# Performance work log

Measured on AMD Instinct MI355X. Metric: run time of the kernel, lower is better.

The kernel has to match this reference:

```python
import jax, jax.numpy as jnp
import numpy as np

T_TOK, N_UNITS, E, H, L_PATH, N_PATHS, B, VOCAB = 16, 4096, 128, 128, 32, 1024, 8, 16384
MAX_PATH_LEN = 32
PAD_ID = 0


def _run_lstm(x, Wi, Wh, b):
    # x: [T, N, E]; torch gate order i, f, g, o
    Hh = Wh.shape[1]
    h0 = jnp.zeros((x.shape[1], Hh), x.dtype)
    def step(carry, xt):
        h, c = carry
        g = xt @ Wi.T + h @ Wh.T + b
        i, f, gg, o = jnp.split(g, 4, axis=-1)
        c = jax.nn.sigmoid(f) * c + jax.nn.sigmoid(i) * jnp.tanh(gg)
        h = jax.nn.sigmoid(o) * jnp.tanh(c)
        return (h, c), h
    _, ys = jax.lax.scan(step, (h0, h0), x)
    return ys


def _bilstm(x, lengths, Wif, Whf, bf, Wib, Whb, bb):
    # emulates pack_padded_sequence + bidirectional LSTM + pad_packed (zeros past length)
    T = x.shape[0]
    t = jnp.arange(T)[:, None]
    valid = t < lengths[None, :]
    out_f = _run_lstm(x, Wif, Whf, bf)
    rev = jnp.clip(lengths[None, :] - 1 - t, 0, T - 1)  # reverse within each valid prefix
    x_rev = jnp.take_along_axis(x, rev[:, :, None], axis=0)
    out_b = jnp.take_along_axis(_run_lstm(x_rev, Wib, Whb, bb), rev[:, :, None], axis=0)
    return jnp.concatenate([out_f, out_b], axis=-1) * valid[:, :, None]


def _layernorm(x, g, b):
    m = x.mean(-1, keepdims=True)
    v = ((x - m) ** 2).mean(-1, keepdims=True)
    return (x - m) * jax.lax.rsqrt(v + 1e-5) * g + b


def _forward(units, paths, unit_per_data, path_per_data, emb, tl_Wif, tl_Whf, tl_bf,
             tl_Wib, tl_Whb, tl_bb, lin_W, lin_b, ln_g, ln_b, attn_w, attn_b,
             pl_Wif, pl_Whf, pl_bf, pl_Wib, pl_Whb, pl_bb, ul_W, ul_b):
    # ---- _token_encoder ----
    is_pad = units == PAD_ID
    tok_len = jnp.where(is_pad.any(0), jnp.argmax(is_pad, 0), units.shape[0])
    x = emb[units]                                              # [T, NU, E]
    h = _bilstm(x, tok_len, tl_Wif, tl_Whf, tl_bf, tl_Wib, tl_Whb, tl_bb)  # [T, NU, 2H]
    out = h @ lin_W.T + lin_b                                   # [T, NU, E]
    q = jnp.tanh(_layernorm(out, ln_g, ln_b))
    scores = q @ attn_w.T + attn_b                              # [T, NU, 1] local attention
    scores = jnp.where(is_pad[:, :, None], -1e9, scores)
    w = jax.nn.softmax(scores, axis=0)
    tok_feat = jnp.einsum('tn,tne->ne', w[..., 0], out)         # [NU, E]
    # ---- _unit_to_path (vectorized ragged gather) ----
    Lp, Pn = paths.shape
    has_end = (paths == -1).any(0)
    fe = jnp.where(has_end, jnp.argmax(paths == -1, 0), Lp)
    ML = min(Lp, MAX_PATH_LEN)
    nb = unit_per_data.shape[0]
    data_of_path = jnp.repeat(jnp.arange(nb), path_per_data, total_repeat_length=Pn)
    u_off = jnp.cumsum(unit_per_data) - unit_per_data
    off_p = u_off[data_of_path]
    un_p = unit_per_data[data_of_path]
    pL = paths[:ML]
    t = jnp.arange(ML)[:, None]
    within = t < fe[None, :]
    keep = within & (pL >= 0) & (pL < un_p[None, :])
    gidx = jnp.clip(jnp.clip(pL, 0, None) + off_p[None, :], 0, tok_feat.shape[0] - 1)
    feats = tok_feat[gidx] * keep[:, :, None]                   # [ML, P, E]
    mask = jnp.where(within, (pL < 0) | (pL > un_p[None, :]), True)
    # ---- _path_encoder ----
    p_len = jnp.where(mask.any(0), jnp.argmax(mask, 0), ML)
    hp = _bilstm(feats, p_len, pl_Wif, pl_Whf, pl_bf, pl_Wib, pl_Whb, pl_bb)
    return hp @ ul_W.T + ul_b                                   # [ML, P, E]


def setup_inputs() -> dict:
    rng = np.random.default_rng(0)
    tok_len = rng.integers(4, T_TOK + 1, N_UNITS); tok_len[0] = T_TOK
    units = rng.integers(1, VOCAB, (T_TOK, N_UNITS))
    units = np.where(np.arange(T_TOK)[:, None] < tok_len[None, :], units, PAD_ID)
    upd = N_UNITS // B
    p_len = rng.integers(8, L_PATH + 1, N_PATHS); p_len[0] = L_PATH
    paths = rng.integers(0, upd, (L_PATH, N_PATHS))
    paths = np.where(np.arange(L_PATH)[:, None] < p_len[None, :], paths, -1)
    key = jax.random.key(0)
    ks = iter(jax.random.split(key, 24))
    def pn(shape, s=0.08):
        return (jax.random.normal(next(ks), shape) * s).astype(jnp.float32)
    return dict(
        units=jnp.asarray(units, jnp.int32),
        paths=jnp.asarray(paths, jnp.int32),
        unit_per_data=jnp.full((B,), upd, jnp.int32),
        path_per_data=jnp.full((B,), N_PATHS // B, jnp.int32),
        emb=pn((VOCAB, E)),
        tl_Wif=pn((4 * H, E)), tl_Whf=pn((4 * H, H)), tl_bf=pn((4 * H,)),
        tl_Wib=pn((4 * H, E)), tl_Whb=pn((4 * H, H)), tl_bb=pn((4 * H,)),
        lin_W=pn((E, 2 * H)), lin_b=pn((E,)),
        ln_g=jnp.ones((E,), jnp.float32), ln_b=jnp.zeros((E,), jnp.float32),
        attn_w=pn((1, E)), attn_b=pn((1,)),
        pl_Wif=pn((4 * H, E)), pl_Whf=pn((4 * H, H)), pl_bf=pn((4 * H,)),
        pl_Wib=pn((4 * H, E)), pl_Whb=pn((4 * H, H)), pl_bb=pn((4 * H,)),
        ul_W=pn((E, 2 * H)), ul_b=pn((E,)),
    )


def reference(units, paths, unit_per_data, path_per_data, emb, tl_Wif, tl_Whf, tl_bf,
              tl_Wib, tl_Whb, tl_bb, lin_W, lin_b, ln_g, ln_b, attn_w, attn_b,
              pl_Wif, pl_Whf, pl_bf, pl_Wib, pl_Whb, pl_bb, ul_W, ul_b):
    return _forward(units, paths, unit_per_data, path_per_data, emb, tl_Wif, tl_Whf, tl_bf,
                    tl_Wib, tl_Whb, tl_bb, lin_W, lin_b, ln_g, ln_b, attn_w, attn_b,
                    pl_Wif, pl_Whf, pl_bf, pl_Wib, pl_Whb, pl_bb, ul_W, ul_b)
```

## Files before the change

### kernel.cpp

```cpp
#include <hip/hip_runtime.h>
#include <cstdint>
#include <cstddef>

#define T_TOKN 16
#define NUNITS 4096
#define LPATH  32
#define NPATHS 1024
#define BNUM   8

typedef __attribute__((ext_vector_type(8))) short short8;
typedef __attribute__((ext_vector_type(4))) short short4x;
typedef __attribute__((ext_vector_type(4))) float f32x4;

enum : size_t {
  OFF_WFRAG   = 0,
  OFF_LINFRAG = 262144,
  OFF_OUTF    = 294912,
  OFF_OUTB    = OFF_OUTF + 4194304,
  OFF_OUTLIN  = OFF_OUTB + 4194304,
  OFF_SCORES  = OFF_OUTLIN + 8388608,
  OFF_TOKFEAT = OFF_SCORES + 65536,
  OFF_POUTF   = OFF_TOKFEAT + 524288,
  OFF_POUTB   = OFF_POUTF + 2097152,
  OFF_INT     = OFF_POUTB + 2097152,
  WS_FLOATS   = OFF_INT + 8192
};

static __device__ __forceinline__ unsigned short f2bf(float f) {
  union { float f; unsigned u; } v; v.f = f;
  unsigned r = v.u + 0x7fffu + ((v.u >> 16) & 1u);
  return (unsigned short)(r >> 16);
}
static __device__ __forceinline__ float bf2f(unsigned short u) {
  union { unsigned u; float f; } v; v.u = ((unsigned)u) << 16;
  return v.f;
}
static __device__ __forceinline__ float sigf(float x)      { return 1.f / (1.f + __expf(-x)); }
static __device__ __forceinline__ float tanhfast(float x)  { return 2.f / (1.f + __expf(-2.f * x)) - 1.f; }

__global__ void prep_kernel(
    const float* __restrict__ tWif, const float* __restrict__ tWhf,
    const float* __restrict__ tWib, const float* __restrict__ tWhb,
    const float* __restrict__ pWif, const float* __restrict__ pWhf,
    const float* __restrict__ pWib, const float* __restrict__ pWhb,
    const float* __restrict__ linW, const float* __restrict__ ulW,
    const int* __restrict__ units, const int* __restrict__ paths,
    const int* __restrict__ upd, const int* __restrict__ ppd,
    float* __restrict__ ws, int* __restrict__ ip)
{
  int idx = blockIdx.x * 256 + threadIdx.x;
  if (idx < 65536) {
    unsigned short* wf = (unsigned short*)(ws + OFF_WFRAG);
    int k8 = idx & 31, g = (idx >> 5) & 511, mat = idx >> 14;
    const float* Wi; const float* Wh;
    switch (mat) {
      case 0: Wi = tWif; Wh = tWhf; break;
      case 1: Wi = tWib; Wh = tWhb; break;
      case 2: Wi = pWif; Wh = pWhf; break;
      default: Wi = pWib; Wh = pWhb; break;
    }
    int kb = k8 << 3;
    const float* sp = (kb < 128) ? (Wi + g * 128 + kb) : (Wh + g * 128 + (kb - 128));
    float4 a = *(const float4*)sp;
    float4 b = *(const float4*)(sp + 4);
    int wvp = g >> 6, ct = (g >> 4) & 3, cl = g & 15;
    int ks = k8 >> 2, quad = k8 & 3;
    size_t base = ((size_t)mat << 17) +
                  (size_t)(((((wvp * 8 + ks) * 4 + ct) * 64) + quad * 16 + cl) << 3);
    short8 o;
    o[0] = (short)f2bf(a.x); o[1] = (short)f2bf(a.y);
    o[2] = (short)f2bf(a.z); o[3] = (short)f2bf(a.w);
    o[4] = (short)f2bf(b.x); o[5] = (short)f2bf(b.y);
    o[6] = (short)f2bf(b.z); o[7] = (short)f2bf(b.w);
    *(short8*)&wf[base] = o;
  } else if (idx < 65536 + 8192) {
    unsigned short* lf = (unsigned short*)(ws + OFF_LINFRAG);
    int j = idx - 65536;
    int k8 = j & 31, e = (j >> 5) & 127, mat = j >> 12;
    const float* W = mat ? ulW : linW;
    int kb = k8 << 3;
    const float* sp = W + e * 256 + kb;
    float4 a = *(const float4*)sp;
    float4 b = *(const float4*)(sp + 4);
    int ct = e >> 4, cl = e & 15;
    int ks = k8 >> 2, quad = k8 & 3;
    size_t base = ((size_t)mat << 15) +
                  (size_t)((((ct * 8 + ks) * 64) + quad * 16 + cl) << 3);
    short8 o;
    o[0] = (short)f2bf(a.x); o[1] = (short)f2bf(a.y);
    o[2] = (short)f2bf(a.z); o[3] = (short)f2bf(a.w);
    o[4] = (short)f2bf(b.x); o[5] = (short)f2bf(b.y);
    o[6] = (short)f2bf(b.z); o[7] = (short)f2bf(b.w);
    *(short8*)&lf[base] = o;
  } else if (idx < 73728 + 4096) {
    int n = idx - 73728;
    int len = T_TOKN;
    for (int t = 0; t < T_TOKN; ++t)
      if (units[t * NUNITS + n] == 0) { len = t; break; }
    ip[n] = len;
  } else if (idx < 77824 + 1024) {
    int p = idx - 77824;
    int* fe_a  = ip + 4096;
    int* p_len = ip + 5120;
    int* off_p = ip + 6144;
    int* un_p  = ip + 7168;
    int cum = 0; int d = BNUM - 1;
    for (int dd = 0; dd < BNUM; ++dd) {
      int c2 = cum + ppd[dd];
      if (p < c2) { d = dd; break; }
      cum = c2;
    }
    int off = 0;
    for (int dd = 0; dd < d; ++dd) off += upd[dd];
    int un = upd[d];
    off_p[p] = off; un_p[p] = un;
    int f = LPATH;
    for (int t = 0; t < LPATH; ++t)
      if (paths[t * NPATHS + p] == -1) { f = t; break; }
    fe_a[p] = f;
    int pl = LPATH;
    for (int t = 0; t < LPATH; ++t) {
      int v = paths[t * NPATHS + p];
      if ((t >= f) || (v < 0) || (v > un)) { pl = t; break; }
    }
    p_len[p] = pl;
  }
}

template <int MODE>
__global__ __launch_bounds__(1024, 4) void lstm_kernel(
    const unsigned short* __restrict__ wfragAll,
    const float* __restrict__ biasF, const float* __restrict__ biasB,
    const float* __restrict__ src,
    const int* __restrict__ idxsrc,
    const int* __restrict__ lens,
    const int* __restrict__ fe_a, const int* __restrict__ off_p, const int* __restrict__ un_p,
    unsigned short* __restrict__ outF, unsigned short* __restrict__ outB)
{
  constexpr int NN   = MODE ? NPATHS : NUNITS;
  constexpr int TT   = MODE ? LPATH : T_TOKN;
  constexpr int M    = MODE ? 8 : 32;
  constexpr int MR   = MODE ? 16 : 32;
  constexpr int NRT  = MR / 16;
  constexpr int ASTR = 264;
  constexpr int USTR = MODE ? 17 : 36;

  __shared__ unsigned short ash[MR * ASTR];
  __shared__ float gatesT[512 * USTR];
  __shared__ int   idxL[M * TT];

  int tid  = threadIdx.x;
  int dir  = blockIdx.y;
  int n0   = blockIdx.x * M;
  int lane = tid & 63, wv = tid >> 6;
  int cl   = lane & 15, quad = lane >> 4;

  const unsigned short* wbase =
      wfragAll + (size_t)((MODE ? 2 : 0) + dir) * 131072;
  int wv8 = wv >> 1;
  short8 bfr[8][2];
#pragma unroll
  for (int ks = 0; ks < 8; ++ks)
#pragma unroll
    for (int c2 = 0; c2 < 2; ++c2) {
      int ct = ((wv & 1) << 1) | c2;
      bfr[ks][c2] = *(const short8*)&wbase[((((wv8 * 8 + ks) * 4 + ct) * 64) + lane) * 8];
    }

  if (MODE == 0) {
    for (int i = tid; i < MR * 128; i += 1024)
      ash[(i >> 7) * ASTR + 128 + (i & 127)] = 0;
  } else {
    for (int i = tid; i < MR * ASTR; i += 1024) ash[i] = 0;
  }
  for (int i = tid; i < M * TT; i += 1024) {
    int u = i / TT, tt = i - u * TT;
    idxL[i] = idxsrc[tt * NN + (n0 + u)];
  }

  const float* bcp = dir ? biasB : biasF;
  const int jj  = tid & 127;
  const int ug  = tid >> 7;
  float bq[4];
#pragma unroll
  for (int q = 0; q < 4; ++q) bq[q] = bcp[q * 128 + jj];
  constexpr int NU = MODE ? 1 : 4;
  float cst[NU];
  int   ulen[NU];
#pragma unroll
  for (int i = 0; i < NU; ++i) {
    cst[i] = 0.f;
    ulen[i] = lens[n0 + ug * NU + i];
  }

  int gu, gk0;
  if (MODE == 0) { gu = tid >> 5; gk0 = (tid & 31) * 4; }
  else           { gu = tid >> 7; gk0 = tid & 127; }
  int gn = n0 + gu;
  int glen = lens[gn];
  int gfe = 0, goff = 0, gun = 0;
  if (MODE) { gfe = fe_a[gn]; goff = off_p[gn]; gun = un_p[gn]; }

  float4 xq; float xs;
  __syncthreads();

  {
    int tau = dir ? min(max(glen - 1, 0), TT - 1) : 0;
    int v = idxL[gu * TT + tau];
    if (MODE == 0) {
      xq = *(const float4*)&src[(size_t)v * 128 + gk0];
    } else {
      bool keep = (tau < gfe) && (v >= 0) && (v < gun);
      xs = keep ? src[(size_t)min(v + goff, NUNITS - 1) * 128 + gk0] : 0.f;
    }
  }
  if (MODE == 0) {
    short4x x4;
    x4[0] = (short)f2bf(xq.x); x4[1] = (short)f2bf(xq.y);
    x4[2] = (short)f2bf(xq.z); x4[3] = (short)f2bf(xq.w);
    *(short4x*)&ash[gu * ASTR + gk0] = x4;
  } else {
    ash[gu * ASTR + gk0] = f2bf(xs);
  }
  __syncthreads();

#pragma unroll 1
  for (int t = 0; t < TT; ++t) {
    {
      int tn = (t + 1 < TT) ? t + 1 : t;
      int taun = dir ? min(max(glen - 1 - tn, 0), TT - 1) : tn;
      int vn = idxL[gu * TT + taun];
      f32x4 acc[NRT][2];
#pragma unroll
      for (int rt = 0; rt < NRT; ++rt)
#pragma unroll
        for (int c2 = 0; c2 < 2; ++c2) {
          f32x4 z = {0.f, 0.f, 0.f, 0.f};
          acc[rt][c2] = z;
        }
#pragma unroll
      for (int ks = 0; ks < 8; ++ks) {
        short8 afr[NRT];
#pragma unroll
        for (int rt = 0; rt < NRT; ++rt)
          afr[rt] = *(const short8*)&ash[(rt * 16 + cl) * ASTR + ks * 32 + (quad << 3)];
#pragma unroll
        for (int rt = 0; rt < NRT; ++rt)
#pragma unroll
          for (int c2 = 0; c2 < 2; ++c2)
            acc[rt][c2] = __builtin_amdgcn_mfma_f32_16x16x32_bf16(
                afr[rt], bfr[ks][c2], acc[rt][c2], 0, 0, 0);
      }
      if (MODE == 0) {
        xq = *(const float4*)&src[(size_t)vn * 128 + gk0];
      } else {
        bool keep = (taun < gfe) && (vn >= 0) && (vn < gun);
        xs = keep ? src[(size_t)min(vn + goff, NUNITS - 1) * 128 + gk0] : 0.f;
      }
      if constexpr (MODE == 0) {
#pragma unroll
        for (int rt = 0; rt < NRT; ++rt)
#pragma unroll
          for (int c2 = 0; c2 < 2; ++c2) {
            int g = wv * 32 + c2 * 16 + cl;
            *(f32x4*)&gatesT[g * USTR + rt * 16 + (quad << 2)] = acc[rt][c2];
          }
      } else {
#pragma unroll
        for (int c2 = 0; c2 < 2; ++c2) {
          int g = wv * 32 + c2 * 16 + cl;
#pragma unroll
          for (int r = 0; r < 4; ++r)
            gatesT[g * USTR + (quad << 2) + r] = acc[0][c2][r];
        }
      }
    }
    __syncthreads();

    if constexpr (MODE == 0) {
      f32x4 gq0 = *(const f32x4*)&gatesT[(0 * 128 + jj) * USTR + (ug << 2)];
      f32x4 gq1 = *(const f32x4*)&gatesT[(1 * 128 + jj) * USTR + (ug << 2)];
      f32x4 gq2 = *(const f32x4*)&gatesT[(2 * 128 + jj) * USTR + (ug << 2)];
      f32x4 gq3 = *(const f32x4*)&gatesT[(3 * 128 + jj) * USTR + (ug << 2)];
#pragma unroll
      for (int r = 0; r < 4; ++r) {
        int u = (ug << 2) + r, n = n0 + u, L = ulen[r];
        if (t < L) {
          float iv = sigf(gq0[r] + bq[0]);
          float fv = sigf(gq1[r] + bq[1]);
          float gv = tanhfast(gq2[r] + bq[2]);
          float ov = sigf(gq3[r] + bq[3]);
          float c = fv * cst[r] + iv * gv;
          cst[r] = c;
          unsigned short hb = f2bf(ov * tanhfast(c));
          ash[u * ASTR + 128 + jj] = hb;
          if (dir == 0) outF[((size_t)t * NN + n) * 128 + jj] = hb;
          else          outB[((size_t)(L - 1 - t) * NN + n) * 128 + jj] = hb;
        } else {
          if (dir == 0) outF[((size_t)t * NN + n) * 128 + jj] = 0;
          else          outB[((size_t)t * NN + n) * 128 + jj] = 0;
        }
      }
    } else {
      int u = ug, n = n0 + u, L = ulen[0];
      if (t < L) {
        float p0 = gatesT[(0 * 128 + jj) * USTR + u] + bq[0];
        float p1 = gatesT[(1 * 128 + jj) * USTR + u] + bq[1];
        float p2 = gatesT[(2 * 128 + jj) * USTR + u] + bq[2];
        float p3 = gatesT[(3 * 128 + jj) * USTR + u] + bq[3];
        float ig = sigf(p0), fg = sigf(p1), gg = tanhfast(p2), og = sigf(p3);
        float c = fg * cst[0] + ig * gg;
        cst[0] = c;
        unsigned short hb = f2bf(og * tanhfast(c));
        ash[u * ASTR + 128 + jj] = hb;
        if (dir == 0) outF[((size_t)t * NN + n) * 128 + jj] = hb;
        else          outB[((size_t)(L - 1 - t) * NN + n) * 128 + jj] = hb;
      } else {
        if (dir == 0) outF[((size_t)t * NN + n) * 128 + jj] = 0;
        else          outB[((size_t)t * NN + n) * 128 + jj] = 0;
      }
    }
    if (t + 1 < TT) {
      if (MODE == 0) {
        short4x x4;
        x4[0] = (short)f2bf(xq.x); x4[1] = (short)f2bf(xq.y);
        x4[2] = (short)f2bf(xq.z); x4[3] = (short)f2bf(xq.w);
        *(short4x*)&ash[gu * ASTR + gk0] = x4;
      } else {
        ash[gu * ASTR + gk0] = f2bf(xs);
      }
    }
    __syncthreads();
  }
}

template <int EPI>
__global__ __launch_bounds__(256) void gemm_mfma(
    const unsigned short* __restrict__ INf, const unsigned short* __restrict__ INb,
    const int* __restrict__ lens,
    const unsigned short* __restrict__ Bfrag, const float* __restrict__ bias,
    void* __restrict__ OUTv, float* __restrict__ scores,
    const float* __restrict__ lng, const float* __restrict__ lnb,
    const float* __restrict__ attw, const float* __restrict__ attb,
    const int* __restrict__ units, int Nn)
{
  constexpr int OSTR = 132;
  __shared__ float outs[64 * OSTR];
  __shared__ float red1[256];
  __shared__ float red2[256];
  __shared__ float rowm[64], rowr[64];
  __shared__ float awsh[128], lgsh[128], lbsh[128];

  int tid = threadIdx.x, lane = tid & 63, wv = tid >> 6;
  int row0 = blockIdx.x * 64;
  int t = row0 / Nn, n0 = row0 % Nn;

  if (EPI == 1 && tid < 128) {
    awsh[tid] = attw[tid]; lgsh[tid] = lng[tid]; lbsh[tid] = lnb[tid];
  }

  short8 bfr[8][2];
#pragma unroll
  for (int ks = 0; ks < 8; ++ks)
#pragma unroll
    for (int c2 = 0; c2 < 2; ++c2) {
      int ct = wv * 2 + c2;
      bfr[ks][c2] = *(const short8*)&Bfrag[(((ct * 8 + ks) * 64) + lane) * 8];
    }

  int rb = lane & 15;
  int koq = (lane >> 4) << 3;
  bool val[4];
#pragma unroll
  for (int rt = 0; rt < 4; ++rt)
    val[rt] = (EPI == 1) ? true : (t < lens[n0 + rt * 16 + rb]);

  f32x4 acc[4][2];
#pragma unroll
  for (int rt = 0; rt < 4; ++rt)
#pragma unroll
    for (int c2 = 0; c2 < 2; ++c2) {
      f32x4 z = {0.f, 0.f, 0.f, 0.f};
      acc[rt][c2] = z;
    }

#pragma unroll
  for (int ks = 0; ks < 8; ++ks) {
    const unsigned short* P = (ks < 4) ? INf : INb;
    int koff = (ks & 3) * 32 + koq;
#pragma unroll
    for (int rt = 0; rt < 4; ++rt) {
      short8 a = {0, 0, 0, 0, 0, 0, 0, 0};
      if (val[rt])
        a = *(const short8*)&P[((size_t)(row0 + rt * 16 + rb)) * 128 + koff];
#pragma unroll
      for (int c2 = 0; c2 < 2; ++c2)
        acc[rt][c2] = __builtin_amdgcn_mfma_f32_16x16x32_bf16(
            a, bfr[ks][c2], acc[rt][c2], 0, 0, 0);
    }
  }

  float bc[2];
#pragma unroll
  for (int c2 = 0; c2 < 2; ++c2) bc[c2] = bias[wv * 32 + c2 * 16 + rb];
#pragma unroll
  for (int rt = 0; rt < 4; ++rt)
#pragma unroll
    for (int c2 = 0; c2 < 2; ++c2) {
      int col = wv * 32 + c2 * 16 + rb;
      int ub  = rt * 16 + ((lane >> 4) << 2);
#pragma unroll
      for (int r = 0; r < 4; ++r)
        outs[(ub + r) * OSTR + col] = acc[rt][c2][r] + bc[c2];
    }
  __syncthreads();

  int row = tid >> 2, seg = tid & 3;
  const float* rp = &outs[row * OSTR + seg * 32];
  size_t go = ((size_t)(row0 + row)) * 128 + seg * 32;

  if (EPI == 0) {
    float* OUT = (float*)OUTv;
#pragma unroll
    for (int x = 0; x < 8; ++x)
      *(f32x4*)&OUT[go + x * 4] = *(const f32x4*)&rp[x * 4];
  } else {
    unsigned short* OUT = (unsigned short*)OUTv;
    f32x4 v[8];
    float s = 0.f, s2 = 0.f;
#pragma unroll
    for (int x = 0; x < 8; ++x) {
      v[x] = *(const f32x4*)&rp[x * 4];
#pragma unroll
      for (int c = 0; c < 4; ++c) { s += v[x][c]; s2 += v[x][c] * v[x][c]; }
    }
    red1[tid] = s; red2[tid] = s2;
    __syncthreads();
    if (tid < 64) {
      float a = red1[tid * 4] + red1[tid * 4 + 1] + red1[tid * 4 + 2] + red1[tid * 4 + 3];
      float b = red2[tid * 4] + red2[tid * 4 + 1] + red2[tid * 4 + 2] + red2[tid * 4 + 3];
      float m = a * (1.f / 128.f);
      float var = b * (1.f / 128.f) - m * m;
      rowm[tid] = m;
      rowr[tid] = rsqrtf(var + 1e-5f);
    }
    __syncthreads();
    float m = rowm[row], rs = rowr[row];
    float sp = 0.f;
#pragma unroll
    for (int x = 0; x < 8; ++x) {
      short4x pv;
#pragma unroll
      for (int c = 0; c < 4; ++c) {
        int col = seg * 32 + x * 4 + c;
        float q = tanhfast((v[x][c] - m) * rs * lgsh[col] + lbsh[col]);
        sp += q * awsh[col];
        pv[c] = (short)f2bf(v[x][c]);
      }
      *(short4x*)&OUT[go + x * 4] = pv;
    }
    red1[tid] = sp;
    __syncthreads();
    if (tid < 64) {
      float s3 = red1[tid * 4] + red1[tid * 4 + 1] + red1[tid * 4 + 2] + red1[tid * 4 + 3]
               + attb[0];
      int n = n0 + tid;
      if (units[t * NUNITS + n] == 0) s3 = -1e9f;
      scores[t * NUNITS + n] = s3;
    }
  }
}

__global__ __launch_bounds__(128) void softmax_feat_kernel(
    const float* __restrict__ scores, const unsigned short* __restrict__ out_lin,
    float* __restrict__ tok_feat)
{
  int n = blockIdx.x;
  int e = threadIdx.x;
  float s[T_TOKN];
  float m = -1e30f;
#pragma unroll
  for (int t = 0; t < T_TOKN; ++t) { s[t] = scores[t * NUNITS + n]; m = fmaxf(m, s[t]); }
  float sum = 0.f;
#pragma unroll
  for (int t = 0; t < T_TOKN; ++t) { s[t] = expf(s[t] - m); sum += s[t]; }
  float inv = 1.f / sum;
  float a = 0.f;
#pragma unroll
  for (int t = 0; t < T_TOKN; ++t)
    a += s[t] * inv * bf2f(out_lin[((size_t)t * NUNITS + n) * 128 + e]);
  tok_feat[n * 128 + e] = a;
}

extern "C" void kernel_launch(void* const* d_in, const int* in_sizes, int n_in,
                              void* d_out, int out_size, void* d_ws, size_t ws_size,
                              hipStream_t stream)
{
  const int*   units = (const int*)d_in[0];
  const int*   paths = (const int*)d_in[1];
  const int*   upd   = (const int*)d_in[2];
  const int*   ppd   = (const int*)d_in[3];
  const float* emb   = (const float*)d_in[4];
  const float* tWif  = (const float*)d_in[5];
  const float* tWhf  = (const float*)d_in[6];
  const float* tbf   = (const float*)d_in[7];
  const float* tWib  = (const float*)d_in[8];
  const float* tWhb  = (const float*)d_in[9];
  const float* tbb   = (const float*)d_in[10];
  const float* linW  = (const float*)d_in[11];
  const float* linb  = (const float*)d_in[12];
  const float* lng   = (const float*)d_in[13];
  const float* lnb   = (const float*)d_in[14];
  const float* attw  = (const float*)d_in[15];
  const float* attb  = (const float*)d_in[16];
  const float* pWif  = (const float*)d_in[17];
  const float* pWhf  = (const float*)d_in[18];
  const float* pbf   = (const float*)d_in[19];
  const float* pWib  = (const float*)d_in[20];
  const float* pWhb  = (const float*)d_in[21];
  const float* pbb   = (const float*)d_in[22];
  const float* ulW   = (const float*)d_in[23];
  const float* ulb   = (const float*)d_in[24];

  float* ws = (float*)d_ws;
  int*   ip = (int*)(ws + OFF_INT);
  if (ws_size < WS_FLOATS * sizeof(float)) return;

  unsigned short* wfrag   = (unsigned short*)(ws + OFF_WFRAG);
  unsigned short* linfrag = (unsigned short*)(ws + OFF_LINFRAG);
  unsigned short* ulfrag  = linfrag + 32768;
  unsigned short* OUTF  = (unsigned short*)(ws + OFF_OUTF);
  unsigned short* OUTB  = (unsigned short*)(ws + OFF_OUTB);
  unsigned short* POUTF = (unsigned short*)(ws + OFF_POUTF);
  unsigned short* POUTB = (unsigned short*)(ws + OFF_POUTB);

  prep_kernel<<<308, 256, 0, stream>>>(tWif, tWhf, tWib, tWhb,
                                       pWif, pWhf, pWib, pWhb,
                                       linW, ulW, units, paths, upd, ppd,
                                       ws, ip);

  lstm_kernel<0><<<dim3(128, 2), 1024, 0, stream>>>(
      wfrag, tbf, tbb, emb, units, ip , nullptr, nullptr, nullptr,
      OUTF, OUTB);

  gemm_mfma<1><<<1024, 256, 0, stream>>>(
      OUTF, OUTB, ip , linfrag, linb,
      (void*)(ws + OFF_OUTLIN), ws + OFF_SCORES, lng, lnb, attw, attb, units, NUNITS);

  softmax_feat_kernel<<<4096, 128, 0, stream>>>(
      ws + OFF_SCORES, (const unsigned short*)(ws + OFF_OUTLIN),
      ws + OFF_TOKFEAT);

  lstm_kernel<1><<<dim3(128, 2), 1024, 0, stream>>>(
      wfrag, pbf, pbb, ws + OFF_TOKFEAT, paths, ip + 5120 ,
      ip + 4096 , ip + 6144 , ip + 7168 ,
      POUTF, POUTB);

  gemm_mfma<0><<<512, 256, 0, stream>>>(
      POUTF, POUTB, ip + 5120 , ulfrag, ulb,
      (void*)d_out, nullptr, nullptr, nullptr, nullptr, nullptr, nullptr, NPATHS);
}
```

Measured before the change: 307.6 us.

## Sort sequences by length and stop each LSTM block at its longest sequence

Adds a counting-sort kernel that orders units and paths by descending length. Each LSTM block now handles a contiguous run of sorted sequences and loops only up to the longest length in that run, so padded timesteps are no longer computed. The backward direction walks blocks in reverse to balance load. The change also halves the sequences per block to double the grid, reworks the gate buffer layout, and drops the explicit zero writes past each length; the token-stage GEMM now masks by length instead. The cost is worse MFMA row utilisation per block, especially for paths, where 4 real rows fill a 16-row tile.

```diff
diff --git a/kernel.cpp b/kernel.cpp
--- a/kernel.cpp
+++ b/kernel.cpp
@@ -23,7 +23,7 @@
   OFF_POUTF   = OFF_TOKFEAT + 524288,
   OFF_POUTB   = OFF_POUTF + 2097152,
   OFF_INT     = OFF_POUTB + 2097152,
-  WS_FLOATS   = OFF_INT + 8192
+  WS_FLOATS   = OFF_INT + 16384
 };
 
 static __device__ __forceinline__ unsigned short f2bf(float f) {
@@ -34,6 +34,9 @@
 static __device__ __forceinline__ float bf2f(unsigned short u) {
   union { unsigned u; float f; } v; v.u = ((unsigned)u) << 16;
   return v.f;
+}
+static __device__ __forceinline__ unsigned pack_bf(float a, float b) {
+  return (unsigned)f2bf(a) | ((unsigned)f2bf(b) << 16);
 }
 static __device__ __forceinline__ float sigf(float x)      { return 1.f / (1.f + __expf(-x)); }
 static __device__ __forceinline__ float tanhfast(float x)  { return 2.f / (1.f + __expf(-2.f * x)) - 1.f; }
@@ -127,6 +130,47 @@
   }
 }
 
+__global__ __launch_bounds__(1024) void sort_kernel(
+    const int* __restrict__ ip, int* __restrict__ uorder, int* __restrict__ porder)
+{
+  __shared__ int cnt[33], base_[33];
+  int tid = threadIdx.x;
+  if (blockIdx.x == 0) {
+    if (tid < 33) cnt[tid] = 0;
+    __syncthreads();
+    for (int n = tid; n < NUNITS; n += 1024)
+      atomicAdd(&cnt[T_TOKN - ip[n]], 1);
+    __syncthreads();
+    if (tid == 0) {
+      int s = 0;
+      for (int b = 0; b < 33; ++b) { base_[b] = s; s += cnt[b]; cnt[b] = 0; }
+    }
+    __syncthreads();
+    for (int n = tid; n < NUNITS; n += 1024) {
+      int b = T_TOKN - ip[n];
+      int pos = base_[b] + atomicAdd(&cnt[b], 1);
+      uorder[pos] = n;
+    }
+  } else {
+    const int* pl = ip + 5120;
+    if (tid < 33) cnt[tid] = 0;
+    __syncthreads();
+    for (int p = tid; p < NPATHS; p += 1024)
+      atomicAdd(&cnt[LPATH - pl[p]], 1);
+    __syncthreads();
+    if (tid == 0) {
+      int s = 0;
+      for (int b = 0; b < 33; ++b) { base_[b] = s; s += cnt[b]; cnt[b] = 0; }
+    }
+    __syncthreads();
+    for (int p = tid; p < NPATHS; p += 1024) {
+      int b = LPATH - pl[p];
+      int pos = base_[b] + atomicAdd(&cnt[b], 1);
+      porder[pos] = p;
+    }
+  }
+}
+
 template <int MODE>
 __global__ __launch_bounds__(1024, 4) void lstm_kernel(
     const unsigned short* __restrict__ wfragAll,
@@ -134,24 +178,24 @@
     const float* __restrict__ src,
     const int* __restrict__ idxsrc,
     const int* __restrict__ lens,
+    const int* __restrict__ order,
     const int* __restrict__ fe_a, const int* __restrict__ off_p, const int* __restrict__ un_p,
     unsigned short* __restrict__ outF, unsigned short* __restrict__ outB)
 {
   constexpr int NN   = MODE ? NPATHS : NUNITS;
   constexpr int TT   = MODE ? LPATH : T_TOKN;
-  constexpr int M    = MODE ? 8 : 32;
-  constexpr int MR   = MODE ? 16 : 32;
-  constexpr int NRT  = MR / 16;
+  constexpr int M    = MODE ? 4 : 16;
   constexpr int ASTR = 264;
-  constexpr int USTR = MODE ? 17 : 36;
-
-  __shared__ unsigned short ash[MR * ASTR];
-  __shared__ float gatesT[512 * USTR];
+  constexpr int GSTR = 514;
+
+  __shared__ unsigned short ash[16 * ASTR];
+  __shared__ float gates[16 * GSTR];
   __shared__ int   idxL[M * TT];
 
   int tid  = threadIdx.x;
   int dir  = blockIdx.y;
-  int n0   = blockIdx.x * M;
+  int rank = dir ? ((int)gridDim.x - 1 - (int)blockIdx.x) : (int)blockIdx.x;
+  int n0   = rank * M;
   int lane = tid & 63, wv = tid >> 6;
   int cl   = lane & 15, quad = lane >> 4;
 
@@ -168,167 +212,127 @@
     }
 
   if (MODE == 0) {
-    for (int i = tid; i < MR * 128; i += 1024)
+    for (int i = tid; i < 16 * 128; i += 1024)
       ash[(i >> 7) * ASTR + 128 + (i & 127)] = 0;
   } else {
-    for (int i = tid; i < MR * ASTR; i += 1024) ash[i] = 0;
+    for (int i = tid; i < 16 * ASTR; i += 1024) ash[i] = 0;
   }
   for (int i = tid; i < M * TT; i += 1024) {
     int u = i / TT, tt = i - u * TT;
-    idxL[i] = idxsrc[tt * NN + (n0 + u)];
-  }
+    idxL[i] = idxsrc[tt * NN + order[n0 + u]];
+  }
+
+  const int TT_run = lens[order[n0]];
 
   const float* bcp = dir ? biasB : biasF;
-  const int jj  = tid & 127;
-  const int ug  = tid >> 7;
-  float bq[4];
-#pragma unroll
-  for (int q = 0; q < 4; ++q) bq[q] = bcp[q * 128 + jj];
-  constexpr int NU = MODE ? 1 : 4;
-  float cst[NU];
-  int   ulen[NU];
-#pragma unroll
-  for (int i = 0; i < NU; ++i) {
-    cst[i] = 0.f;
-    ulen[i] = lens[n0 + ug * NU + i];
-  }
+  int j2 = MODE ? (tid & 127) : ((tid & 63) * 2);
+  int ug = MODE ? (tid >> 7)  : (tid >> 6);
+  bool pw_act = MODE ? (ug < M) : true;
+  float2 b2[4];
+#pragma unroll
+  for (int q = 0; q < 4; ++q) {
+    if (MODE == 0) b2[q] = *(const float2*)&bcp[q * 128 + j2];
+    else           b2[q] = make_float2(bcp[q * 128 + j2], 0.f);
+  }
+  int pun = order[n0 + (pw_act ? ug : 0)];
+  int pL  = lens[pun];
+  float cstA = 0.f, cstB = 0.f;
 
   int gu, gk0;
-  if (MODE == 0) { gu = tid >> 5; gk0 = (tid & 31) * 4; }
+  if (MODE == 0) { gu = tid >> 6; gk0 = (tid & 63) * 2; }
   else           { gu = tid >> 7; gk0 = tid & 127; }
-  int gn = n0 + gu;
+  bool g_act = MODE ? (gu < M) : true;
+  int gn = order[n0 + (g_act ? gu : 0)];
   int glen = lens[gn];
   int gfe = 0, goff = 0, gun = 0;
   if (MODE) { gfe = fe_a[gn]; goff = off_p[gn]; gun = un_p[gn]; }
 
-  float4 xq; float xs;
+  float2 xq; float xs;
   __syncthreads();
 
-  {
+  if (g_act) {
     int tau = dir ? min(max(glen - 1, 0), TT - 1) : 0;
     int v = idxL[gu * TT + tau];
     if (MODE == 0) {
-      xq = *(const float4*)&src[(size_t)v * 128 + gk0];
+      xq = *(const float2*)&src[(size_t)v * 128 + gk0];
+      *(unsigned*)&ash[gu * ASTR + gk0] = pack_bf(xq.x, xq.y);
     } else {
       bool keep = (tau < gfe) && (v >= 0) && (v < gun);
       xs = keep ? src[(size_t)min(v + goff, NUNITS - 1) * 128 + gk0] : 0.f;
-    }
-  }
-  if (MODE == 0) {
-    short4x x4;
-    x4[0] = (short)f2bf(xq.x); x4[1] = (short)f2bf(xq.y);
-    x4[2] = (short)f2bf(xq.z); x4[3] = (short)f2bf(xq.w);
-    *(short4x*)&ash[gu * ASTR + gk0] = x4;
-  } else {
-    ash[gu * ASTR + gk0] = f2bf(xs);
+      ash[gu * ASTR + gk0] = f2bf(xs);
+    }
   }
   __syncthreads();
 
 #pragma unroll 1
-  for (int t = 0; t < TT; ++t) {
+  for (int t = 0; t < TT_run; ++t) {
     {
-      int tn = (t + 1 < TT) ? t + 1 : t;
+      int tn = (t + 1 < TT_run) ? t + 1 : t;
       int taun = dir ? min(max(glen - 1 - tn, 0), TT - 1) : tn;
-      int vn = idxL[gu * TT + taun];
-      f32x4 acc[NRT][2];
-#pragma unroll
-      for (int rt = 0; rt < NRT; ++rt)
-#pragma unroll
-        for (int c2 = 0; c2 < 2; ++c2) {
-          f32x4 z = {0.f, 0.f, 0.f, 0.f};
-          acc[rt][c2] = z;
-        }
+      int vn = g_act ? idxL[gu * TT + taun] : 0;
+      f32x4 acc0 = {0.f, 0.f, 0.f, 0.f}, acc1 = {0.f, 0.f, 0.f, 0.f};
 #pragma unroll
       for (int ks = 0; ks < 8; ++ks) {
-        short8 afr[NRT];
-#pragma unroll
-        for (int rt = 0; rt < NRT; ++rt)
-          afr[rt] = *(const short8*)&ash[(rt * 16 + cl) * ASTR + ks * 32 + (quad << 3)];
-#pragma unroll
-        for (int rt = 0; rt < NRT; ++rt)
-#pragma unroll
-          for (int c2 = 0; c2 < 2; ++c2)
-            acc[rt][c2] = __builtin_amdgcn_mfma_f32_16x16x32_bf16(
-                afr[rt], bfr[ks][c2], acc[rt][c2], 0, 0, 0);
+        short8 afr = *(const short8*)&ash[cl * ASTR + ks * 32 + (quad << 3)];
+        acc0 = __builtin_amdgcn_mfma_f32_16x16x32_bf16(afr, bfr[ks][0], acc0, 0, 0, 0);
+        acc1 = __builtin_amdgcn_mfma_f32_16x16x32_bf16(afr, bfr[ks][1], acc1, 0, 0, 0);
       }
-      if (MODE == 0) {
-        xq = *(const float4*)&src[(size_t)vn * 128 + gk0];
-      } else {
-        bool keep = (taun < gfe) && (vn >= 0) && (vn < gun);
-        xs = keep ? src[(size_t)min(vn + goff, NUNITS - 1) * 128 + gk0] : 0.f;
-      }
-      if constexpr (MODE == 0) {
-#pragma unroll
-        for (int rt = 0; rt < NRT; ++rt)
-#pragma unroll
-          for (int c2 = 0; c2 < 2; ++c2) {
-            int g = wv * 32 + c2 * 16 + cl;
-            *(f32x4*)&gatesT[g * USTR + rt * 16 + (quad << 2)] = acc[rt][c2];
-          }
-      } else {
-#pragma unroll
-        for (int c2 = 0; c2 < 2; ++c2) {
-          int g = wv * 32 + c2 * 16 + cl;
-#pragma unroll
-          for (int r = 0; r < 4; ++r)
-            gatesT[g * USTR + (quad << 2) + r] = acc[0][c2][r];
+      if (g_act) {
+        if (MODE == 0) {
+          xq = *(const float2*)&src[(size_t)vn * 128 + gk0];
+        } else {
+          bool keep = (taun < gfe) && (vn >= 0) && (vn < gun);
+          xs = keep ? src[(size_t)min(vn + goff, NUNITS - 1) * 128 + gk0] : 0.f;
         }
       }
-    }
-    __syncthreads();
-
-    if constexpr (MODE == 0) {
-      f32x4 gq0 = *(const f32x4*)&gatesT[(0 * 128 + jj) * USTR + (ug << 2)];
-      f32x4 gq1 = *(const f32x4*)&gatesT[(1 * 128 + jj) * USTR + (ug << 2)];
-      f32x4 gq2 = *(const f32x4*)&gatesT[(2 * 128 + jj) * USTR + (ug << 2)];
-      f32x4 gq3 = *(const f32x4*)&gatesT[(3 * 128 + jj) * USTR + (ug << 2)];
-#pragma unroll
-      for (int r = 0; r < 4; ++r) {
-        int u = (ug << 2) + r, n = n0 + u, L = ulen[r];
-        if (t < L) {
-          float iv = sigf(gq0[r] + bq[0]);
-          float fv = sigf(gq1[r] + bq[1]);
-          float gv = tanhfast(gq2[r] + bq[2]);
-          float ov = sigf(gq3[r] + bq[3]);
-          float c = fv * cst[r] + iv * gv;
-          cst[r] = c;
-          unsigned short hb = f2bf(ov * tanhfast(c));
-          ash[u * ASTR + 128 + jj] = hb;
-          if (dir == 0) outF[((size_t)t * NN + n) * 128 + jj] = hb;
-          else          outB[((size_t)(L - 1 - t) * NN + n) * 128 + jj] = hb;
-        } else {
-          if (dir == 0) outF[((size_t)t * NN + n) * 128 + jj] = 0;
-          else          outB[((size_t)t * NN + n) * 128 + jj] = 0;
+      {
+        int g = wv * 32 + cl;
+        int ub = quad << 2;
+#pragma unroll
+        for (int r = 0; r < 4; ++r) {
+          gates[(ub + r) * GSTR + g]      = acc0[r];
+          gates[(ub + r) * GSTR + g + 16] = acc1[r];
         }
       }
-    } else {
-      int u = ug, n = n0 + u, L = ulen[0];
-      if (t < L) {
-        float p0 = gatesT[(0 * 128 + jj) * USTR + u] + bq[0];
-        float p1 = gatesT[(1 * 128 + jj) * USTR + u] + bq[1];
-        float p2 = gatesT[(2 * 128 + jj) * USTR + u] + bq[2];
-        float p3 = gatesT[(3 * 128 + jj) * USTR + u] + bq[3];
-        float ig = sigf(p0), fg = sigf(p1), gg = tanhfast(p2), og = sigf(p3);
-        float c = fg * cst[0] + ig * gg;
-        cst[0] = c;
+    }
+    __syncthreads();
+
+    if (pw_act && t < pL) {
+      if (MODE == 0) {
+        const float* gg = gates + ug * GSTR + j2;
+        float2 g0 = *(const float2*)(gg);
+        float2 g1 = *(const float2*)(gg + 128);
+        float2 g2 = *(const float2*)(gg + 256);
+        float2 g3 = *(const float2*)(gg + 384);
+        float i0 = sigf(g0.x + b2[0].x), i1 = sigf(g0.y + b2[0].y);
+        float f0 = sigf(g1.x + b2[1].x), f1 = sigf(g1.y + b2[1].y);
+        float c0 = tanhfast(g2.x + b2[2].x), c1 = tanhfast(g2.y + b2[2].y);
+        float o0 = sigf(g3.x + b2[3].x), o1 = sigf(g3.y + b2[3].y);
+        float cA = f0 * cstA + i0 * c0;
+        float cB = f1 * cstB + i1 * c1;
+        cstA = cA; cstB = cB;
+        unsigned hp = pack_bf(o0 * tanhfast(cA), o1 * tanhfast(cB));
+        *(unsigned*)&ash[ug * ASTR + 128 + j2] = hp;
+        if (dir == 0) *(unsigned*)&outF[((size_t)t * NN + pun) * 128 + j2] = hp;
+        else          *(unsigned*)&outB[((size_t)(pL - 1 - t) * NN + pun) * 128 + j2] = hp;
+      } else {
+        const float* gg = gates + ug * GSTR + j2;
+        float p0 = gg[0]   + b2[0].x;
+        float p1 = gg[128] + b2[1].x;
+        float p2 = gg[256] + b2[2].x;
+        float p3 = gg[384] + b2[3].x;
+        float ig = sigf(p0), fg = sigf(p1), gg2 = tanhfast(p2), og = sigf(p3);
+        float c = fg * cstA + ig * gg2;
+        cstA = c;
         unsigned short hb = f2bf(og * tanhfast(c));
-        ash[u * ASTR + 128 + jj] = hb;
-        if (dir == 0) outF[((size_t)t * NN + n) * 128 + jj] = hb;
-        else          outB[((size_t)(L - 1 - t) * NN + n) * 128 + jj] = hb;
-      } else {
-        if (dir == 0) outF[((size_t)t * NN + n) * 128 + jj] = 0;
-        else          outB[((size_t)t * NN + n) * 128 + jj] = 0;
+        ash[ug * ASTR + 128 + j2] = hb;
+        if (dir == 0) outF[((size_t)t * NN + pun) * 128 + j2] = hb;
+        else          outB[((size_t)(pL - 1 - t) * NN + pun) * 128 + j2] = hb;
       }
     }
-    if (t + 1 < TT) {
-      if (MODE == 0) {
-        short4x x4;
-        x4[0] = (short)f2bf(xq.x); x4[1] = (short)f2bf(xq.y);
-        x4[2] = (short)f2bf(xq.z); x4[3] = (short)f2bf(xq.w);
-        *(short4x*)&ash[gu * ASTR + gk0] = x4;
-      } else {
-        ash[gu * ASTR + gk0] = f2bf(xs);
-      }
+    if (g_act && t + 1 < TT_run) {
+      if (MODE == 0) *(unsigned*)&ash[gu * ASTR + gk0] = pack_bf(xq.x, xq.y);
+      else           ash[gu * ASTR + gk0] = f2bf(xs);
     }
     __syncthreads();
   }
@@ -373,7 +377,7 @@
   bool val[4];
 #pragma unroll
   for (int rt = 0; rt < 4; ++rt)
-    val[rt] = (EPI == 1) ? true : (t < lens[n0 + rt * 16 + rb]);
+    val[rt] = (t < lens[n0 + rt * 16 + rb]);
 
   f32x4 acc[4][2];
 #pragma unroll
@@ -533,15 +537,19 @@
   unsigned short* OUTB  = (unsigned short*)(ws + OFF_OUTB);
   unsigned short* POUTF = (unsigned short*)(ws + OFF_POUTF);
   unsigned short* POUTB = (unsigned short*)(ws + OFF_POUTB);
+  int* uorder = ip + 8192;
+  int* porder = ip + 12288;
 
   prep_kernel<<<308, 256, 0, stream>>>(tWif, tWhf, tWib, tWhb,
                                        pWif, pWhf, pWib, pWhb,
                                        linW, ulW, units, paths, upd, ppd,
                                        ws, ip);
 
-  lstm_kernel<0><<<dim3(128, 2), 1024, 0, stream>>>(
-      wfrag, tbf, tbb, emb, units, ip , nullptr, nullptr, nullptr,
-      OUTF, OUTB);
+  sort_kernel<<<2, 1024, 0, stream>>>(ip, uorder, porder);
+
+  lstm_kernel<0><<<dim3(256, 2), 1024, 0, stream>>>(
+      wfrag, tbf, tbb, emb, units, ip , uorder,
+      nullptr, nullptr, nullptr, OUTF, OUTB);
 
   gemm_mfma<1><<<1024, 256, 0, stream>>>(
       OUTF, OUTB, ip , linfrag, linb,
@@ -551,8 +559,8 @@
       ws + OFF_SCORES, (const unsigned short*)(ws + OFF_OUTLIN),
       ws + OFF_TOKFEAT);
 
-  lstm_kernel<1><<<dim3(128, 2), 1024, 0, stream>>>(
-      wfrag, pbf, pbb, ws + OFF_TOKFEAT, paths, ip + 5120 ,
+  lstm_kernel<1><<<dim3(256, 2), 1024, 0, stream>>>(
+      wfrag, pbf, pbb, ws + OFF_TOKFEAT, paths, ip + 5120 , porder,
       ip + 4096 , ip + 6144 , ip + 7168 ,
       POUTF, POUTB);
 
```

New measurement: 350.4 us. 1.14x slower.
